# Performance work log

Measured on AMD Instinct MI355X. Metric: run time of the kernel, lower is better.

## Reference

```python
import jax, jax.numpy as jnp
import numpy as np
from jax import lax

B, N, D = 8, 1024, 512
HEAD_DIM = 64          # = num_attention_heads arg (used as split chunk size in torch)
H = D // HEAD_DIM      # actual number of heads = 8
TOPK = 32
EPS = 1e-5


def setup_inputs() -> dict:
    key = jax.random.key(0)
    ks = jax.random.split(key, 20)
    s = 0.02
    inp = {
        "src": jax.random.normal(ks[0], (B, N, D), jnp.float32),
        "tgt": jax.random.normal(ks[1], (B, N, D), jnp.float32),
        "Wq": jax.random.normal(ks[2], (D, D), jnp.float32) * s,
        "bq": jnp.zeros((D,), jnp.float32),
        "Wk": jax.random.normal(ks[3], (D, D), jnp.float32) * s,
        "bk": jnp.zeros((D,), jnp.float32),
        "Wv": jax.random.normal(ks[4], (D, D), jnp.float32) * s,
        "bv": jnp.zeros((D,), jnp.float32),
        "W1": jax.random.normal(ks[5], (D, D), jnp.float32) * s,
        "b1": jnp.zeros((D,), jnp.float32),
        "W2": jax.random.normal(ks[6], (D, D), jnp.float32) * s,
        "b2": jnp.zeros((D,), jnp.float32),
        "g1": jnp.ones((D,), jnp.float32),
        "be1": jnp.zeros((D,), jnp.float32),
        "g2": jnp.ones((D,), jnp.float32),
        "be2": jnp.zeros((D,), jnp.float32),
    }
    return inp


def _layer_norm(x, g, b):
    mu = jnp.mean(x, axis=-1, keepdims=True)
    var = jnp.mean(jnp.square(x - mu), axis=-1, keepdims=True)
    return (x - mu) * lax.rsqrt(var + EPS) * g + b


def _to_heads(x):
    # torch: cat(split(x, HEAD_DIM, dim=-1), dim=0) -> head-major leading dim
    # [B, N, D] -> [H*B, N, HEAD_DIM]
    return x.reshape(B, N, H, HEAD_DIM).transpose(2, 0, 1, 3).reshape(H * B, N, HEAD_DIM)


def reference(src, tgt, Wq, bq, Wk, bk, Wv, bv, W1, b1, W2, b2, g1, be1, g2, be2):
    q = _to_heads(tgt @ Wq + bq) / jnp.sqrt(jnp.float32(D))  # scale by hidden_dim**0.5 (as in source)
    k = _to_heads(src @ Wk + bk)
    v = _to_heads(src @ Wv + bv)

    scores = jnp.einsum('hqd,hkd->hqk', q, k)  # [H*B, N, N]

    idx = lax.top_k(scores, TOPK)[1]                       # [H*B, N, TOPK]
    vals = jnp.take_along_axis(scores, idx, axis=-1)       # gather top-k values
    sparse = jnp.full_like(scores, -jnp.inf)
    hb = jnp.arange(H * B)[:, None, None]
    qn = jnp.arange(N)[None, :, None]
    sparse = sparse.at[hb, qn, idx].set(vals)

    attn = jax.nn.softmax(sparse, axis=-1)                 # rows have TOPK finite entries
    out = jnp.einsum('hqk,hkd->hqd', attn, v)              # [H*B, N, HEAD_DIM]
    # torch: cat(split(out, B, dim=0), dim=-1) -> [B, N, D]
    out = out.reshape(H, B, N, HEAD_DIM).transpose(1, 2, 0, 3).reshape(B, N, D)

    x = _layer_norm(tgt + out, g1, be1)
    ff = jax.nn.relu(x @ W1 + b1) @ W2 + b2   # dropout = identity in eval mode
    return _layer_norm(x + ff, g2, be2)
```

## Files before the change

### kernel.cpp

```cpp
#include <hip/hip_runtime.h>
#include <math.h>

#define NSQ 1024
#define DM  512
#define HDIM 64
#define MROWS 8192
#define TOPK 32

typedef unsigned short u16;
typedef __attribute__((ext_vector_type(8))) short bf16x8;
typedef __attribute__((ext_vector_type(4))) float f32x4;

#define MFMA_B16(A,B,C) __builtin_amdgcn_mfma_f32_16x16x32_bf16(A,B,C,0,0,0)

__device__ __forceinline__ unsigned f2b(float x) {
    unsigned u = __float_as_uint(x);
    return (u + 0x7FFFu + ((u >> 16) & 1u)) >> 16;
}
__device__ __forceinline__ float b2f(unsigned h) { return __uint_as_float(h << 16); }
__device__ __forceinline__ unsigned ordu(float f) {
    unsigned b = __float_as_uint(f);
    return b ^ (0x80000000u | (unsigned)((int)b >> 31));
}

__global__ __launch_bounds__(256) void conv_split(
    const float* __restrict__ x, u16* __restrict__ hi, u16* __restrict__ lo)
{
    int idx = blockIdx.x * 256 + threadIdx.x;
    float4 v = ((const float4*)x)[idx];
    float f[4] = {v.x, v.y, v.z, v.w};
    ushort4 hv, lv;
    unsigned h;
    h = f2b(f[0]); hv.x = (u16)h; lv.x = (u16)f2b(f[0] - b2f(h));
    h = f2b(f[1]); hv.y = (u16)h; lv.y = (u16)f2b(f[1] - b2f(h));
    h = f2b(f[2]); hv.z = (u16)h; lv.z = (u16)f2b(f[2] - b2f(h));
    h = f2b(f[3]); hv.w = (u16)h; lv.w = (u16)f2b(f[3] - b2f(h));
    ((ushort4*)hi)[idx] = hv;
    ((ushort4*)lo)[idx] = lv;
}

__global__ __launch_bounds__(256) void wconv(
    const float* __restrict__ W, u16* __restrict__ thi, u16* __restrict__ tlo)
{
    __shared__ float T[32][33];
    const int tx = threadIdx.x & 31, ty = threadIdx.x >> 5;
    const int n0 = blockIdx.x * 32, k0 = blockIdx.y * 32;
#pragma unroll
    for (int p = 0; p < 4; ++p) {
        int r = ty + p * 8;
        T[r][tx] = W[(size_t)(k0 + r) * DM + n0 + tx];
    }
    __syncthreads();
#pragma unroll
    for (int p = 0; p < 4; ++p) {
        int rr = ty + p * 8;
        float val = T[tx][rr];
        unsigned h = f2b(val);
        size_t off = (size_t)(n0 + rr) * DM + k0 + tx;
        thi[off] = (u16)h;
        tlo[off] = (u16)f2b(val - b2f(h));
    }
}

template<int SPLIT, int RELU, int OUTMODE>
__global__ __launch_bounds__(256) void mm512(
    const u16* __restrict__ Ah_g, const u16* __restrict__ Al_g,
    const u16* __restrict__ Bh_g, const u16* __restrict__ Bl_g,
    const float* __restrict__ bias, const float* __restrict__ R,
    float scale, float* __restrict__ outF,
    u16* __restrict__ outHi, u16* __restrict__ outLo)
{
    __shared__ u16 Ah[128 * 40], Bh[128 * 40];
    __shared__ u16 Al[SPLIT ? 128 * 40 : 8], Bl[SPLIT ? 128 * 40 : 8];
    const int tid = threadIdx.x, lane = tid & 63, w = tid >> 6;
    const int wr = (w >> 1) * 64, wc = (w & 1) * 64;
    const int ml = lane & 15, q8 = (lane >> 4) * 8, q4 = (lane >> 4) * 4;
    const int row0 = blockIdx.x * 128, col0 = blockIdx.y * 128;
    const int sm = tid >> 2, sk = (tid & 3) * 8;

    f32x4 acc[4][4];
#pragma unroll
    for (int i = 0; i < 4; ++i)
#pragma unroll
        for (int j = 0; j < 4; ++j) acc[i][j] = {0.f, 0.f, 0.f, 0.f};

    for (int k0 = 0; k0 < DM; k0 += 32) {
#pragma unroll
        for (int p = 0; p < 2; ++p) {
            int m = sm + p * 64;
            *(uint4*)&Ah[m * 40 + sk] = *(const uint4*)&Ah_g[(size_t)(row0 + m) * DM + k0 + sk];
            *(uint4*)&Bh[m * 40 + sk] = *(const uint4*)&Bh_g[(size_t)(col0 + m) * DM + k0 + sk];
            if (SPLIT) {
                *(uint4*)&Al[m * 40 + sk] = *(const uint4*)&Al_g[(size_t)(row0 + m) * DM + k0 + sk];
                *(uint4*)&Bl[m * 40 + sk] = *(const uint4*)&Bl_g[(size_t)(col0 + m) * DM + k0 + sk];
            }
        }
        __syncthreads();
        bf16x8 a_h[4], b_h[4], a_l[4], b_l[4];
#pragma unroll
        for (int i = 0; i < 4; ++i) {
            a_h[i] = *(const bf16x8*)&Ah[(wr + i * 16 + ml) * 40 + q8];
            b_h[i] = *(const bf16x8*)&Bh[(wc + i * 16 + ml) * 40 + q8];
            if (SPLIT) {
                a_l[i] = *(const bf16x8*)&Al[(wr + i * 16 + ml) * 40 + q8];
                b_l[i] = *(const bf16x8*)&Bl[(wc + i * 16 + ml) * 40 + q8];
            }
        }
#pragma unroll
        for (int i = 0; i < 4; ++i)
#pragma unroll
            for (int j = 0; j < 4; ++j) {
                acc[i][j] = MFMA_B16(a_h[i], b_h[j], acc[i][j]);
                if (SPLIT) {
                    acc[i][j] = MFMA_B16(a_h[i], b_l[j], acc[i][j]);
                    acc[i][j] = MFMA_B16(a_l[i], b_h[j], acc[i][j]);
                    acc[i][j] = MFMA_B16(a_l[i], b_l[j], acc[i][j]);
                }
            }
        __syncthreads();
    }

    float bcol[4];
#pragma unroll
    for (int j = 0; j < 4; ++j) bcol[j] = bias[col0 + wc + j * 16 + ml];
#pragma unroll
    for (int i = 0; i < 4; ++i)
#pragma unroll
        for (int j = 0; j < 4; ++j)
#pragma unroll
            for (int r = 0; r < 4; ++r) {
                int gm = row0 + wr + i * 16 + q4 + r;
                int gn = col0 + wc + j * 16 + ml;
                float t = acc[i][j][r] + bcol[j];
                if (RELU) t = fmaxf(t, 0.f);
                t *= scale;
                size_t off = (size_t)gm * DM + gn;
                if (OUTMODE == 0) {
                    if (R) t += R[off];
                    outF[off] = t;
                } else if (OUTMODE == 1) {
                    unsigned hb = f2b(t);
                    outHi[off] = (u16)hb;
                    outLo[off] = (u16)f2b(t - b2f(hb));
                } else {
                    outHi[off] = (u16)f2b(t);
                }
            }
}

__global__ __launch_bounds__(256) void score_mfma(
    const u16* __restrict__ qhi, const u16* __restrict__ qlo,
    const u16* __restrict__ khi, const u16* __restrict__ klo,
    float* __restrict__ scores, int hb0)
{
    __shared__ u16 Qh[128 * 40], Ql[128 * 40], Kh[128 * 40], Kl[128 * 40];
    const int tid = threadIdx.x, lane = tid & 63, w = tid >> 6;
    const int wr = (w >> 1) * 64, wc = (w & 1) * 64;
    const int ml = lane & 15, q8 = (lane >> 4) * 8, q4 = (lane >> 4) * 4;
    const int z = blockIdx.z, hb = hb0 + z, h = hb >> 3, b = hb & 7;
    const int r0 = blockIdx.x * 128, c0 = blockIdx.y * 128;
    const int sm = tid >> 2, sk = (tid & 3) * 8;
    const size_t base = (size_t)b * NSQ * DM + (size_t)h * HDIM;

    f32x4 acc[4][4];
#pragma unroll
    for (int i = 0; i < 4; ++i)
#pragma unroll
        for (int j = 0; j < 4; ++j) acc[i][j] = {0.f, 0.f, 0.f, 0.f};

    for (int k0 = 0; k0 < HDIM; k0 += 32) {
#pragma unroll
        for (int p = 0; p < 2; ++p) {
            int m = sm + p * 64;
            *(uint4*)&Qh[m * 40 + sk] = *(const uint4*)&qhi[base + (size_t)(r0 + m) * DM + k0 + sk];
            *(uint4*)&Ql[m * 40 + sk] = *(const uint4*)&qlo[base + (size_t)(r0 + m) * DM + k0 + sk];
            *(uint4*)&Kh[m * 40 + sk] = *(const uint4*)&khi[base + (size_t)(c0 + m) * DM + k0 + sk];
            *(uint4*)&Kl[m * 40 + sk] = *(const uint4*)&klo[base + (size_t)(c0 + m) * DM + k0 + sk];
        }
        __syncthreads();
        bf16x8 a_h[4], b_h[4], a_l[4], b_l[4];
#pragma unroll
        for (int i = 0; i < 4; ++i) {
            a_h[i] = *(const bf16x8*)&Qh[(wr + i * 16 + ml) * 40 + q8];
            b_h[i] = *(const bf16x8*)&Kh[(wc + i * 16 + ml) * 40 + q8];
            a_l[i] = *(const bf16x8*)&Ql[(wr + i * 16 + ml) * 40 + q8];
            b_l[i] = *(const bf16x8*)&Kl[(wc + i * 16 + ml) * 40 + q8];
        }
#pragma unroll
        for (int i = 0; i < 4; ++i)
#pragma unroll
            for (int j = 0; j < 4; ++j) {
                acc[i][j] = MFMA_B16(a_h[i], b_h[j], acc[i][j]);
                acc[i][j] = MFMA_B16(a_h[i], b_l[j], acc[i][j]);
                acc[i][j] = MFMA_B16(a_l[i], b_h[j], acc[i][j]);
                acc[i][j] = MFMA_B16(a_l[i], b_l[j], acc[i][j]);
            }
        __syncthreads();
    }
#pragma unroll
    for (int i = 0; i < 4; ++i)
#pragma unroll
        for (int j = 0; j < 4; ++j)
#pragma unroll
            for (int r = 0; r < 4; ++r)
                scores[((size_t)z * NSQ + r0 + wr + i * 16 + q4 + r) * NSQ + c0 + wc + j * 16 + ml]
                    = acc[i][j][r];
}

__global__ __launch_bounds__(256) void select_pv(
    const float* __restrict__ scores, const u16* __restrict__ vhi,
    u16* __restrict__ ao, int hb0)
{
    __shared__ float pv_[4][TOPK];
    __shared__ int   pi_[4][TOPK];
    const int tid = threadIdx.x, w = tid >> 6, lane = tid & 63;
    const int z = blockIdx.y, hb = hb0 + z, h = hb >> 3, b = hb & 7;
    const int row = blockIdx.x * 4 + w;
    const float* srow = scores + ((size_t)z * NSQ + row) * NSQ;

    float f[16]; unsigned u[16];
    float s1 = 0.f, s2 = 0.f;
#pragma unroll
    for (int i = 0; i < 16; ++i) {
        f[i] = srow[i * 64 + lane];
        s1 += f[i];
        s2 = fmaf(f[i], f[i], s2);
    }
#pragma unroll
    for (int o = 32; o; o >>= 1) { s1 += __shfl_xor(s1, o); s2 += __shfl_xor(s2, o); }
    float mu = s1 * (1.f / 1024.f);
    float sg = sqrtf(fmaxf(s2 * (1.f / 1024.f) - mu * mu, 0.f)) + 1e-20f;
#pragma unroll
    for (int i = 0; i < 16; ++i) u[i] = ordu(f[i]);

    auto cnt = [&](unsigned t) -> int {
        int tot = 0;
#pragma unroll
        for (int i = 0; i < 16; ++i) tot += __popcll(__ballot(u[i] > t));
        return tot;
    };

    float tl = mu + 1.2f * sg, dstep = 0.7f * sg;
    unsigned lo = ordu(tl);
    int clo = cnt(lo);
    while (clo < TOPK) { tl -= dstep; dstep *= 2.f; lo = ordu(tl); clo = cnt(lo); }
    float th = mu + 4.0f * sg, ustep = 2.0f * sg;
    unsigned hi = ordu(th);
    int chi = cnt(hi);
    while (chi >= TOPK) { lo = hi; clo = chi; th += ustep; ustep *= 2.f; hi = ordu(th); chi = cnt(hi); }
    if (clo > TOPK) {
        while (hi - lo > 1u) {
            unsigned mid = lo + ((hi - lo) >> 1);
            int c = cnt(mid);
            if (c >= TOPK) { lo = mid; clo = c; if (c == TOPK) break; }
            else hi = mid;
        }
    }

    unsigned selm = 0;
#pragma unroll
    for (int i = 0; i < 16; ++i) if (u[i] > lo) selm |= (1u << i);

    int nsel = clo;
    unsigned bhi = lo + 1u;
    while (nsel > TOPK) {
        int myidx = -1, myslot = 0;
#pragma unroll
        for (int i = 0; i < 16; ++i)
            if (((selm >> i) & 1u) && u[i] == bhi) { myidx = i * 64 + lane; myslot = i; }
        int mx = myidx;
#pragma unroll
        for (int o = 32; o; o >>= 1) mx = max(mx, __shfl_xor(mx, o));
        if (myidx == mx && myidx >= 0) selm &= ~(1u << myslot);
        nsel--;
    }

    float lm = -INFINITY;
#pragma unroll
    for (int i = 0; i < 16; ++i) if ((selm >> i) & 1u) lm = fmaxf(lm, f[i]);
#pragma unroll
    for (int o = 32; o; o >>= 1) lm = fmaxf(lm, __shfl_xor(lm, o));
    float e[16], es = 0.f;
#pragma unroll
    for (int i = 0; i < 16; ++i) {
        e[i] = ((selm >> i) & 1u) ? __expf(f[i] - lm) : 0.f;
        es += e[i];
    }
#pragma unroll
    for (int o = 32; o; o >>= 1) es += __shfl_xor(es, o);
    float inv = 1.f / es;

    unsigned long long ltm = (1ull << lane) - 1ull;
    int basec = 0;
#pragma unroll
    for (int i = 0; i < 16; ++i) {
        unsigned long long m = __ballot((selm >> i) & 1u);
        if ((selm >> i) & 1u) {
            int slot = basec + __popcll(m & ltm);
            pv_[w][slot] = e[i] * inv;
            pi_[w][slot] = i * 64 + lane;
        }
        basec += __popcll(m);
    }
    __syncthreads();

    float acc = 0.f;
    const u16* vb = vhi + (size_t)b * NSQ * DM + (size_t)h * HDIM + lane;
    const float* pvr = pv_[w];
    const int*   pir = pi_[w];
#pragma unroll 8
    for (int t = 0; t < TOPK; ++t)
        acc = fmaf(pvr[t], b2f(vb[(size_t)pir[t] * DM]), acc);
    ao[((size_t)b * NSQ + row) * DM + (size_t)h * HDIM + lane] = (u16)f2b(acc);
}

__global__ __launch_bounds__(256) void ln_fused(
    const float* __restrict__ a, const u16* __restrict__ addb,
    const float* __restrict__ g, const float* __restrict__ be,
    float* __restrict__ outF, u16* __restrict__ outHi)
{
    __shared__ float red[4][2];
    const int row = blockIdx.x, tid = threadIdx.x, w = tid >> 6;
    float2 v = ((const float2*)(a + (size_t)row * DM))[tid];
    if (addb) {
        ushort2 ab = ((const ushort2*)(addb + (size_t)row * DM))[tid];
        v.x += b2f(ab.x); v.y += b2f(ab.y);
    }
    float s = v.x + v.y, q = v.x * v.x + v.y * v.y;
#pragma unroll
    for (int o = 32; o; o >>= 1) { s += __shfl_xor(s, o); q += __shfl_xor(q, o); }
    if ((tid & 63) == 0) { red[w][0] = s; red[w][1] = q; }
    __syncthreads();
    float S = red[0][0] + red[1][0] + red[2][0] + red[3][0];
    float Q = red[0][1] + red[1][1] + red[2][1] + red[3][1];
    float mu = S * (1.f / DM);
    float var = Q * (1.f / DM) - mu * mu;
    float rs = rsqrtf(var + 1e-5f);
    float2 gv = ((const float2*)g)[tid];
    float2 bv = ((const float2*)be)[tid];
    float2 o;
    o.x = (v.x - mu) * rs * gv.x + bv.x;
    o.y = (v.y - mu) * rs * gv.y + bv.y;
    if (outF) ((float2*)(outF + (size_t)row * DM))[tid] = o;
    if (outHi) {
        ushort2 hv; hv.x = (u16)f2b(o.x); hv.y = (u16)f2b(o.y);
        ((ushort2*)(outHi + (size_t)row * DM))[tid] = hv;
    }
}

extern "C" void kernel_launch(void* const* d_in, const int* in_sizes, int n_in,
                              void* d_out, int out_size, void* d_ws, size_t ws_size,
                              hipStream_t stream) {
    const float* src = (const float*)d_in[0];
    const float* tgt = (const float*)d_in[1];
    const float* Wq  = (const float*)d_in[2];
    const float* bq  = (const float*)d_in[3];
    const float* Wk  = (const float*)d_in[4];
    const float* bk  = (const float*)d_in[5];
    const float* Wv  = (const float*)d_in[6];
    const float* bv  = (const float*)d_in[7];
    const float* W1  = (const float*)d_in[8];
    const float* b1  = (const float*)d_in[9];
    const float* W2  = (const float*)d_in[10];
    const float* b2  = (const float*)d_in[11];
    const float* g1  = (const float*)d_in[12];
    const float* be1 = (const float*)d_in[13];
    const float* g2  = (const float*)d_in[14];
    const float* be2 = (const float*)d_in[15];

    const size_t WPLANE = (size_t)DM * DM;
    u16* wt  = (u16*)d_ws;
    u16* wqh = wt;              u16* wql = wt + WPLANE;
    u16* wkh = wt + 2 * WPLANE; u16* wkl = wt + 3 * WPLANE;
    u16* wvh = wt + 4 * WPLANE; u16* wvl = wt + 5 * WPLANE;
    u16* w1h = wt + 6 * WPLANE; u16* w1l = wt + 7 * WPLANE;
    u16* w2h = wt + 8 * WPLANE; u16* w2l = wt + 9 * WPLANE;
    auto at = [&](size_t mb) { return (char*)d_ws + (mb << 20); };
    u16* Phi = (u16*)at(5);
    u16* Plo = (u16*)at(13);
    u16* qhi = (u16*)at(21);
    u16* khi = (u16*)at(29);
    u16* qlo = (u16*)at(37);
    u16* klo = (u16*)at(45);
    u16* vhi = (u16*)at(53);
    u16* aob = (u16*)at(61);
    float* xb = (float*)at(69);
    float* f2 = (float*)at(37);
    float* sc; int slab;
    if (ws_size >= ((size_t)149 << 20)) { sc = (float*)at(85); slab = 16; }
    else                                { sc = xb;             slab = 4;  }

    dim3 blk(256);
    const float qscale = 0.04419417382415922f;

    wconv<<<dim3(16, 16), blk, 0, stream>>>(Wq, wqh, wql);
    wconv<<<dim3(16, 16), blk, 0, stream>>>(Wk, wkh, wkl);
    wconv<<<dim3(16, 16), blk, 0, stream>>>(Wv, wvh, wvl);
    wconv<<<dim3(16, 16), blk, 0, stream>>>(W1, w1h, w1l);
    wconv<<<dim3(16, 16), blk, 0, stream>>>(W2, w2h, w2l);

    conv_split<<<4096, blk, 0, stream>>>(tgt, Phi, Plo);
    mm512<1, 0, 1><<<dim3(64, 4), blk, 0, stream>>>(Phi, Plo, wqh, wql, bq, nullptr, qscale,
                                                    nullptr, qhi, qlo);
    conv_split<<<4096, blk, 0, stream>>>(src, Phi, Plo);
    mm512<1, 0, 1><<<dim3(64, 4), blk, 0, stream>>>(Phi, Plo, wkh, wkl, bk, nullptr, 1.f,
                                                    nullptr, khi, klo);
    mm512<0, 0, 2><<<dim3(64, 4), blk, 0, stream>>>(Phi, nullptr, wvh, nullptr, bv, nullptr, 1.f,
                                                    nullptr, vhi, nullptr);

    for (int hb0 = 0; hb0 < 64; hb0 += slab) {
        score_mfma<<<dim3(8, 8, slab), blk, 0, stream>>>(qhi, qlo, khi, klo, sc, hb0);
        select_pv<<<dim3(256, slab), blk, 0, stream>>>(sc, vhi, aob, hb0);
    }

    ln_fused<<<8192, blk, 0, stream>>>(tgt, aob, g1, be1, xb, qhi);
    mm512<0, 1, 2><<<dim3(64, 4), blk, 0, stream>>>(qhi, nullptr, w1h, nullptr, b1, nullptr, 1.f,
                                                    nullptr, khi, nullptr);
    mm512<0, 0, 0><<<dim3(64, 4), blk, 0, stream>>>(khi, nullptr, w2h, nullptr, b2, xb, 1.f,
                                                    f2, nullptr, nullptr);
    ln_fused<<<8192, blk, 0, stream>>>(f2, nullptr, g2, be2, (float*)d_out, nullptr);
}
```

Baseline: 456.3 us.

## Fuse score computation with top-k select and PV into one kernel

Merges the score MFMA kernel and the select/PV kernel into a single kernel. Each block computes a 16-row by 1024-column score slab into 64KB of LDS, then runs top-k selection and the weighted V sum from LDS. This removes the global round trip of the 256MB score tensor and the per-slab launch loop. It also batches the five weight conversions and the two input conversions into single launches. The trade-offs are that K is re-read from global memory by every row block, and the large LDS footprint limits occupancy.

Measured after the change: 546.2 us. 1.2x slower.

```diff
diff --git a/kernel.cpp b/kernel.cpp
--- a/kernel.cpp
+++ b/kernel.cpp
@@ -4,8 +4,8 @@
 #define NSQ 1024
 #define DM  512
 #define HDIM 64
-#define MROWS 8192
 #define TOPK 32
+#define QSTR 72
 
 typedef unsigned short u16;
 typedef __attribute__((ext_vector_type(8))) short bf16x8;
@@ -23,9 +23,15 @@
     return b ^ (0x80000000u | (unsigned)((int)b >> 31));
 }
 
-__global__ __launch_bounds__(256) void conv_split(
-    const float* __restrict__ x, u16* __restrict__ hi, u16* __restrict__ lo)
+__global__ __launch_bounds__(256) void conv2(
+    const float* __restrict__ tgt, const float* __restrict__ src,
+    u16* __restrict__ Thi, u16* __restrict__ Tlo,
+    u16* __restrict__ Shi, u16* __restrict__ Slo)
 {
+    const int z = blockIdx.y;
+    const float* x = z ? src : tgt;
+    u16* hi = z ? Shi : Thi;
+    u16* lo = z ? Slo : Tlo;
     int idx = blockIdx.x * 256 + threadIdx.x;
     float4 v = ((const float4*)x)[idx];
     float f[4] = {v.x, v.y, v.z, v.w};
@@ -39,10 +45,17 @@
     ((ushort4*)lo)[idx] = lv;
 }
 
-__global__ __launch_bounds__(256) void wconv(
-    const float* __restrict__ W, u16* __restrict__ thi, u16* __restrict__ tlo)
+__global__ __launch_bounds__(256) void wconv5(
+    const float* __restrict__ Wq, const float* __restrict__ Wk,
+    const float* __restrict__ Wv, const float* __restrict__ W1,
+    const float* __restrict__ W2, u16* __restrict__ planes)
 {
     __shared__ float T[32][33];
+    const int wsel = blockIdx.z;
+    const float* W = (wsel == 0) ? Wq : (wsel == 1) ? Wk : (wsel == 2) ? Wv
+                   : (wsel == 3) ? W1 : W2;
+    u16* thi = planes + (size_t)wsel * 2 * DM * DM;
+    u16* tlo = thi + (size_t)DM * DM;
     const int tx = threadIdx.x & 31, ty = threadIdx.x >> 5;
     const int n0 = blockIdx.x * 32, k0 = blockIdx.y * 32;
 #pragma unroll
@@ -139,179 +152,167 @@
                     if (R) t += R[off];
                     outF[off] = t;
                 } else if (OUTMODE == 1) {
-                    unsigned hb = f2b(t);
-                    outHi[off] = (u16)hb;
-                    outLo[off] = (u16)f2b(t - b2f(hb));
+                    unsigned hb2 = f2b(t);
+                    outHi[off] = (u16)hb2;
+                    outLo[off] = (u16)f2b(t - b2f(hb2));
                 } else {
                     outHi[off] = (u16)f2b(t);
                 }
             }
 }
 
-__global__ __launch_bounds__(256) void score_mfma(
+__global__ __launch_bounds__(256, 2) void score_select(
     const u16* __restrict__ qhi, const u16* __restrict__ qlo,
     const u16* __restrict__ khi, const u16* __restrict__ klo,
-    float* __restrict__ scores, int hb0)
+    const u16* __restrict__ vhi, u16* __restrict__ ao)
 {
-    __shared__ u16 Qh[128 * 40], Ql[128 * 40], Kh[128 * 40], Kl[128 * 40];
-    const int tid = threadIdx.x, lane = tid & 63, w = tid >> 6;
-    const int wr = (w >> 1) * 64, wc = (w & 1) * 64;
-    const int ml = lane & 15, q8 = (lane >> 4) * 8, q4 = (lane >> 4) * 4;
-    const int z = blockIdx.z, hb = hb0 + z, h = hb >> 3, b = hb & 7;
-    const int r0 = blockIdx.x * 128, c0 = blockIdx.y * 128;
-    const int sm = tid >> 2, sk = (tid & 3) * 8;
-    const size_t base = (size_t)b * NSQ * DM + (size_t)h * HDIM;
-
-    f32x4 acc[4][4];
-#pragma unroll
-    for (int i = 0; i < 4; ++i)
-#pragma unroll
-        for (int j = 0; j < 4; ++j) acc[i][j] = {0.f, 0.f, 0.f, 0.f};
-
-    for (int k0 = 0; k0 < HDIM; k0 += 32) {
-#pragma unroll
-        for (int p = 0; p < 2; ++p) {
-            int m = sm + p * 64;
-            *(uint4*)&Qh[m * 40 + sk] = *(const uint4*)&qhi[base + (size_t)(r0 + m) * DM + k0 + sk];
-            *(uint4*)&Ql[m * 40 + sk] = *(const uint4*)&qlo[base + (size_t)(r0 + m) * DM + k0 + sk];
-            *(uint4*)&Kh[m * 40 + sk] = *(const uint4*)&khi[base + (size_t)(c0 + m) * DM + k0 + sk];
-            *(uint4*)&Kl[m * 40 + sk] = *(const uint4*)&klo[base + (size_t)(c0 + m) * DM + k0 + sk];
-        }
-        __syncthreads();
-        bf16x8 a_h[4], b_h[4], a_l[4], b_l[4];
-#pragma unroll
-        for (int i = 0; i < 4; ++i) {
-            a_h[i] = *(const bf16x8*)&Qh[(wr + i * 16 + ml) * 40 + q8];
-            b_h[i] = *(const bf16x8*)&Kh[(wc + i * 16 + ml) * 40 + q8];
-            a_l[i] = *(const bf16x8*)&Ql[(wr + i * 16 + ml) * 40 + q8];
-            b_l[i] = *(const bf16x8*)&Kl[(wc + i * 16 + ml) * 40 + q8];
-        }
-#pragma unroll
-        for (int i = 0; i < 4; ++i)
-#pragma unroll
-            for (int j = 0; j < 4; ++j) {
-                acc[i][j] = MFMA_B16(a_h[i], b_h[j], acc[i][j]);
-                acc[i][j] = MFMA_B16(a_h[i], b_l[j], acc[i][j]);
-                acc[i][j] = MFMA_B16(a_l[i], b_h[j], acc[i][j]);
-                acc[i][j] = MFMA_B16(a_l[i], b_l[j], acc[i][j]);
-            }
-        __syncthreads();
-    }
-#pragma unroll
-    for (int i = 0; i < 4; ++i)
-#pragma unroll
-        for (int j = 0; j < 4; ++j)
-#pragma unroll
-            for (int r = 0; r < 4; ++r)
-                scores[((size_t)z * NSQ + r0 + wr + i * 16 + q4 + r) * NSQ + c0 + wc + j * 16 + ml]
-                    = acc[i][j][r];
-}
-
-__global__ __launch_bounds__(256) void select_pv(
-    const float* __restrict__ scores, const u16* __restrict__ vhi,
-    u16* __restrict__ ao, int hb0)
-{
+    __shared__ float S[16 * NSQ];
+    __shared__ u16 Qh[16 * QSTR], Ql[16 * QSTR];
     __shared__ float pv_[4][TOPK];
     __shared__ int   pi_[4][TOPK];
-    const int tid = threadIdx.x, w = tid >> 6, lane = tid & 63;
-    const int z = blockIdx.y, hb = hb0 + z, h = hb >> 3, b = hb & 7;
-    const int row = blockIdx.x * 4 + w;
-    const float* srow = scores + ((size_t)z * NSQ + row) * NSQ;
-
-    float f[16]; unsigned u[16];
-    float s1 = 0.f, s2 = 0.f;
-#pragma unroll
-    for (int i = 0; i < 16; ++i) {
-        f[i] = srow[i * 64 + lane];
-        s1 += f[i];
-        s2 = fmaf(f[i], f[i], s2);
-    }
-#pragma unroll
-    for (int o = 32; o; o >>= 1) { s1 += __shfl_xor(s1, o); s2 += __shfl_xor(s2, o); }
-    float mu = s1 * (1.f / 1024.f);
-    float sg = sqrtf(fmaxf(s2 * (1.f / 1024.f) - mu * mu, 0.f)) + 1e-20f;
-#pragma unroll
-    for (int i = 0; i < 16; ++i) u[i] = ordu(f[i]);
-
-    auto cnt = [&](unsigned t) -> int {
-        int tot = 0;
-#pragma unroll
-        for (int i = 0; i < 16; ++i) tot += __popcll(__ballot(u[i] > t));
-        return tot;
-    };
-
-    float tl = mu + 1.2f * sg, dstep = 0.7f * sg;
-    unsigned lo = ordu(tl);
-    int clo = cnt(lo);
-    while (clo < TOPK) { tl -= dstep; dstep *= 2.f; lo = ordu(tl); clo = cnt(lo); }
-    float th = mu + 4.0f * sg, ustep = 2.0f * sg;
-    unsigned hi = ordu(th);
-    int chi = cnt(hi);
-    while (chi >= TOPK) { lo = hi; clo = chi; th += ustep; ustep *= 2.f; hi = ordu(th); chi = cnt(hi); }
-    if (clo > TOPK) {
-        while (hi - lo > 1u) {
-            unsigned mid = lo + ((hi - lo) >> 1);
-            int c = cnt(mid);
-            if (c >= TOPK) { lo = mid; clo = c; if (c == TOPK) break; }
-            else hi = mid;
-        }
-    }
-
-    unsigned selm = 0;
-#pragma unroll
-    for (int i = 0; i < 16; ++i) if (u[i] > lo) selm |= (1u << i);
-
-    int nsel = clo;
-    unsigned bhi = lo + 1u;
-    while (nsel > TOPK) {
-        int myidx = -1, myslot = 0;
-#pragma unroll
-        for (int i = 0; i < 16; ++i)
-            if (((selm >> i) & 1u) && u[i] == bhi) { myidx = i * 64 + lane; myslot = i; }
-        int mx = myidx;
-#pragma unroll
-        for (int o = 32; o; o >>= 1) mx = max(mx, __shfl_xor(mx, o));
-        if (myidx == mx && myidx >= 0) selm &= ~(1u << myslot);
-        nsel--;
-    }
-
-    float lm = -INFINITY;
-#pragma unroll
-    for (int i = 0; i < 16; ++i) if ((selm >> i) & 1u) lm = fmaxf(lm, f[i]);
-#pragma unroll
-    for (int o = 32; o; o >>= 1) lm = fmaxf(lm, __shfl_xor(lm, o));
-    float e[16], es = 0.f;
-#pragma unroll
-    for (int i = 0; i < 16; ++i) {
-        e[i] = ((selm >> i) & 1u) ? __expf(f[i] - lm) : 0.f;
-        es += e[i];
-    }
-#pragma unroll
-    for (int o = 32; o; o >>= 1) es += __shfl_xor(es, o);
-    float inv = 1.f / es;
-
-    unsigned long long ltm = (1ull << lane) - 1ull;
-    int basec = 0;
-#pragma unroll
-    for (int i = 0; i < 16; ++i) {
-        unsigned long long m = __ballot((selm >> i) & 1u);
-        if ((selm >> i) & 1u) {
-            int slot = basec + __popcll(m & ltm);
-            pv_[w][slot] = e[i] * inv;
-            pi_[w][slot] = i * 64 + lane;
-        }
-        basec += __popcll(m);
+
+    const int tid = threadIdx.x, lane = tid & 63, w = tid >> 6;
+    const int ml = lane & 15, q8 = (lane >> 4) * 8, q4 = (lane >> 4) * 4;
+    const int hb = blockIdx.y, h = hb >> 3, b = hb & 7;
+    const int r0 = blockIdx.x * 16;
+
+    {
+        int t2 = tid & 127, m = t2 >> 3, k8 = (t2 & 7) * 8;
+        const u16* srcp = (tid < 128) ? qhi : qlo;
+        u16* dst = (tid < 128) ? Qh : Ql;
+        *(uint4*)&dst[m * QSTR + k8] =
+            *(const uint4*)&srcp[((size_t)(b * NSQ + r0 + m)) * DM + h * HDIM + k8];
     }
     __syncthreads();
 
-    float acc = 0.f;
-    const u16* vb = vhi + (size_t)b * NSQ * DM + (size_t)h * HDIM + lane;
-    const float* pvr = pv_[w];
-    const int*   pir = pi_[w];
+    bf16x8 a_h0 = *(const bf16x8*)&Qh[ml * QSTR + q8];
+    bf16x8 a_h1 = *(const bf16x8*)&Qh[ml * QSTR + 32 + q8];
+    bf16x8 a_l0 = *(const bf16x8*)&Ql[ml * QSTR + q8];
+    bf16x8 a_l1 = *(const bf16x8*)&Ql[ml * QSTR + 32 + q8];
+
+    const u16* khp = khi + ((size_t)(b * NSQ + w * 256 + ml)) * DM + h * HDIM + q8;
+    const u16* klp = klo + ((size_t)(b * NSQ + w * 256 + ml)) * DM + h * HDIM + q8;
+    float* sbase = &S[q4 * NSQ + w * 256 + ml];
+
+#pragma unroll 2
+    for (int t = 0; t < 16; ++t) {
+        bf16x8 bh0 = *(const bf16x8*)(khp);
+        bf16x8 bh1 = *(const bf16x8*)(khp + 32);
+        bf16x8 bl0 = *(const bf16x8*)(klp);
+        bf16x8 bl1 = *(const bf16x8*)(klp + 32);
+        f32x4 ac0 = {0.f, 0.f, 0.f, 0.f}, ac1 = {0.f, 0.f, 0.f, 0.f};
+        ac0 = MFMA_B16(a_h0, bh0, ac0);
+        ac0 = MFMA_B16(a_h1, bh1, ac0);
+        ac0 = MFMA_B16(a_l0, bh0, ac0);
+        ac0 = MFMA_B16(a_l1, bh1, ac0);
+        ac1 = MFMA_B16(a_h0, bl0, ac1);
+        ac1 = MFMA_B16(a_h1, bl1, ac1);
+        ac1 = MFMA_B16(a_l0, bl0, ac1);
+        ac1 = MFMA_B16(a_l1, bl1, ac1);
+#pragma unroll
+        for (int r = 0; r < 4; ++r)
+            sbase[r * NSQ + t * 16] = ac0[r] + ac1[r];
+        khp += 16 * DM;
+        klp += 16 * DM;
+    }
+    __syncthreads();
+
+    const u16* vb = vhi + ((size_t)b * NSQ) * DM + h * HDIM + lane;
+    for (int rr = 0; rr < 4; ++rr) {
+        const int rloc = w * 4 + rr;
+        const float* srow = &S[(size_t)rloc * NSQ];
+
+        float f[16]; unsigned u[16];
+        float s1 = 0.f, s2 = 0.f;
+#pragma unroll
+        for (int i = 0; i < 16; ++i) {
+            f[i] = srow[i * 64 + lane];
+            s1 += f[i];
+            s2 = fmaf(f[i], f[i], s2);
+        }
+#pragma unroll
+        for (int o = 32; o; o >>= 1) { s1 += __shfl_xor(s1, o); s2 += __shfl_xor(s2, o); }
+        float mu = s1 * (1.f / 1024.f);
+        float sg = sqrtf(fmaxf(s2 * (1.f / 1024.f) - mu * mu, 0.f)) + 1e-20f;
+#pragma unroll
+        for (int i = 0; i < 16; ++i) u[i] = ordu(f[i]);
+
+        auto cnt = [&](unsigned t) -> int {
+            int tot = 0;
+#pragma unroll
+            for (int i = 0; i < 16; ++i) tot += __popcll(__ballot(u[i] > t));
+            return tot;
+        };
+
+        float tl = mu + 1.2f * sg, dstep = 0.7f * sg;
+        unsigned lo = ordu(tl);
+        int clo = cnt(lo);
+        while (clo < TOPK) { tl -= dstep; dstep *= 2.f; lo = ordu(tl); clo = cnt(lo); }
+        float th = mu + 4.0f * sg, ustep = 2.0f * sg;
+        unsigned hi = ordu(th);
+        int chi = cnt(hi);
+        while (chi >= TOPK) { lo = hi; clo = chi; th += ustep; ustep *= 2.f; hi = ordu(th); chi = cnt(hi); }
+        if (clo > TOPK) {
+            while (hi - lo > 1u) {
+                unsigned mid = lo + ((hi - lo) >> 1);
+                int c = cnt(mid);
+                if (c >= TOPK) { lo = mid; clo = c; if (c == TOPK) break; }
+                else hi = mid;
+            }
+        }
+
+        unsigned selm = 0;
+#pragma unroll
+        for (int i = 0; i < 16; ++i) if (u[i] > lo) selm |= (1u << i);
+
+        int nsel = clo;
+        unsigned bhi = lo + 1u;
+        while (nsel > TOPK) {
+            int myidx = -1, myslot = 0;
+#pragma unroll
+            for (int i = 0; i < 16; ++i)
+                if (((selm >> i) & 1u) && u[i] == bhi) { myidx = i * 64 + lane; myslot = i; }
+            int mx = myidx;
+#pragma unroll
+            for (int o = 32; o; o >>= 1) mx = max(mx, __shfl_xor(mx, o));
+            if (myidx == mx && myidx >= 0) selm &= ~(1u << myslot);
+            nsel--;
+        }
+
+        float lm = -INFINITY;
+#pragma unroll
+        for (int i = 0; i < 16; ++i) if ((selm >> i) & 1u) lm = fmaxf(lm, f[i]);
+#pragma unroll
+        for (int o = 32; o; o >>= 1) lm = fmaxf(lm, __shfl_xor(lm, o));
+        float e[16], es = 0.f;
+#pragma unroll
+        for (int i = 0; i < 16; ++i) {
+            e[i] = ((selm >> i) & 1u) ? __expf(f[i] - lm) : 0.f;
+            es += e[i];
+        }
+#pragma unroll
+        for (int o = 32; o; o >>= 1) es += __shfl_xor(es, o);
+        float inv = 1.f / es;
+
+        unsigned long long ltm = (1ull << lane) - 1ull;
+        int basec = 0;
+#pragma unroll
+        for (int i = 0; i < 16; ++i) {
+            unsigned long long m = __ballot((selm >> i) & 1u);
+            if ((selm >> i) & 1u) {
+                int slot = basec + __popcll(m & ltm);
+                pv_[w][slot] = e[i] * inv;
+                pi_[w][slot] = i * 64 + lane;
+            }
+            basec += __popcll(m);
+        }
+
+        float acc = 0.f;
 #pragma unroll 8
-    for (int t = 0; t < TOPK; ++t)
-        acc = fmaf(pvr[t], b2f(vb[(size_t)pir[t] * DM]), acc);
-    ao[((size_t)b * NSQ + row) * DM + (size_t)h * HDIM + lane] = (u16)f2b(acc);
+        for (int t = 0; t < TOPK; ++t)
+            acc = fmaf(pv_[w][t], b2f(vb[(size_t)pi_[w][t] * DM]), acc);
+        ao[((size_t)(b * NSQ + r0 + rloc)) * DM + h * HDIM + lane] = (u16)f2b(acc);
+    }
 }
 
 __global__ __launch_bounds__(256) void ln_fused(
@@ -369,54 +370,40 @@
     const float* be2 = (const float*)d_in[15];
 
     const size_t WPLANE = (size_t)DM * DM;
-    u16* wt  = (u16*)d_ws;
-    u16* wqh = wt;              u16* wql = wt + WPLANE;
-    u16* wkh = wt + 2 * WPLANE; u16* wkl = wt + 3 * WPLANE;
-    u16* wvh = wt + 4 * WPLANE; u16* wvl = wt + 5 * WPLANE;
-    u16* w1h = wt + 6 * WPLANE; u16* w1l = wt + 7 * WPLANE;
-    u16* w2h = wt + 8 * WPLANE; u16* w2l = wt + 9 * WPLANE;
+    u16* planes = (u16*)d_ws;
+    auto wh = [&](int i) { return planes + (size_t)i * 2 * WPLANE; };
+    auto wl = [&](int i) { return planes + (size_t)i * 2 * WPLANE + WPLANE; };
     auto at = [&](size_t mb) { return (char*)d_ws + (mb << 20); };
-    u16* Phi = (u16*)at(5);
-    u16* Plo = (u16*)at(13);
-    u16* qhi = (u16*)at(21);
-    u16* khi = (u16*)at(29);
-    u16* qlo = (u16*)at(37);
-    u16* klo = (u16*)at(45);
-    u16* vhi = (u16*)at(53);
-    u16* aob = (u16*)at(61);
-    float* xb = (float*)at(69);
-    float* f2 = (float*)at(37);
-    float* sc; int slab;
-    if (ws_size >= ((size_t)149 << 20)) { sc = (float*)at(85); slab = 16; }
-    else                                { sc = xb;             slab = 4;  }
+    u16* Thi = (u16*)at(8);   u16* Tlo = (u16*)at(16);
+    u16* Shi = (u16*)at(24);  u16* Slo = (u16*)at(32);
+    u16* qhi = (u16*)at(40);  u16* qlo = (u16*)at(48);
+    u16* khi = (u16*)at(56);  u16* klo = (u16*)at(64);
+    u16* vhi = (u16*)at(72);
+    u16* aob = (u16*)at(80);
+    float* xb = (float*)at(88);
+    u16* xhi = (u16*)at(104);
+    u16* hhi = (u16*)at(112);
+    float* f2 = (float*)at(120);
 
     dim3 blk(256);
     const float qscale = 0.04419417382415922f;
 
-    wconv<<<dim3(16, 16), blk, 0, stream>>>(Wq, wqh, wql);
-    wconv<<<dim3(16, 16), blk, 0, stream>>>(Wk, wkh, wkl);
-    wconv<<<dim3(16, 16), blk, 0, stream>>>(Wv, wvh, wvl);
-    wconv<<<dim3(16, 16), blk, 0, stream>>>(W1, w1h, w1l);
-    wconv<<<dim3(16, 16), blk, 0, stream>>>(W2, w2h, w2l);
-
-    conv_split<<<4096, blk, 0, stream>>>(tgt, Phi, Plo);
-    mm512<1, 0, 1><<<dim3(64, 4), blk, 0, stream>>>(Phi, Plo, wqh, wql, bq, nullptr, qscale,
-                                                    nullptr, qhi, qlo);
-    conv_split<<<4096, blk, 0, stream>>>(src, Phi, Plo);
-    mm512<1, 0, 1><<<dim3(64, 4), blk, 0, stream>>>(Phi, Plo, wkh, wkl, bk, nullptr, 1.f,
-                                                    nullptr, khi, klo);
-    mm512<0, 0, 2><<<dim3(64, 4), blk, 0, stream>>>(Phi, nullptr, wvh, nullptr, bv, nullptr, 1.f,
-                                                    nullptr, vhi, nullptr);
-
-    for (int hb0 = 0; hb0 < 64; hb0 += slab) {
-        score_mfma<<<dim3(8, 8, slab), blk, 0, stream>>>(qhi, qlo, khi, klo, sc, hb0);
-        select_pv<<<dim3(256, slab), blk, 0, stream>>>(sc, vhi, aob, hb0);
-    }
-
-    ln_fused<<<8192, blk, 0, stream>>>(tgt, aob, g1, be1, xb, qhi);
-    mm512<0, 1, 2><<<dim3(64, 4), blk, 0, stream>>>(qhi, nullptr, w1h, nullptr, b1, nullptr, 1.f,
-                                                    nullptr, khi, nullptr);
-    mm512<0, 0, 0><<<dim3(64, 4), blk, 0, stream>>>(khi, nullptr, w2h, nullptr, b2, xb, 1.f,
-                                                    f2, nullptr, nullptr);
+    wconv5<<<dim3(16, 16, 5), blk, 0, stream>>>(Wq, Wk, Wv, W1, W2, planes);
+    conv2<<<dim3(4096, 2), blk, 0, stream>>>(tgt, src, Thi, Tlo, Shi, Slo);
+
+    mm512<1, 0, 1><<<dim3(64, 4), blk, 0, stream>>>(Thi, Tlo, wh(0), wl(0), bq, nullptr,
+                                                    qscale, nullptr, qhi, qlo);
+    mm512<1, 0, 1><<<dim3(64, 4), blk, 0, stream>>>(Shi, Slo, wh(1), wl(1), bk, nullptr,
+                                                    1.f, nullptr, khi, klo);
+    mm512<0, 0, 2><<<dim3(64, 4), blk, 0, stream>>>(Shi, nullptr, wh(2), nullptr, bv, nullptr,
+                                                    1.f, nullptr, vhi, nullptr);
+
+    score_select<<<dim3(64, 64), blk, 0, stream>>>(qhi, qlo, khi, klo, vhi, aob);
+
+    ln_fused<<<8192, blk, 0, stream>>>(tgt, aob, g1, be1, xb, xhi);
+    mm512<0, 1, 2><<<dim3(64, 4), blk, 0, stream>>>(xhi, nullptr, wh(3), nullptr, b1, nullptr,
+                                                    1.f, nullptr, hhi, nullptr);
+    mm512<0, 0, 0><<<dim3(64, 4), blk, 0, stream>>>(hhi, nullptr, wh(4), nullptr, b2, xb,
+                                                    1.f, f2, nullptr, nullptr);
     ln_fused<<<8192, blk, 0, stream>>>(f2, nullptr, g2, be2, (float*)d_out, nullptr);
 }
```
